# Performance work log

Measured on AMD Instinct MI355X. Metric: run time of the kernel, lower is better.

## Reference

```python
import jax, jax.numpy as jnp
import numpy as np

N, E, G = 50000, 800000, 512
IN, HID, H1, H2, OUT = 128, 32, 8, 4, 128
D1, D2 = HID * H1, HID * H2  # 256, 128


def _ln(x, g, b, eps=1e-5):
    m = x.mean(-1, keepdims=True)
    v = jnp.var(x, axis=-1, keepdims=True)
    return (x - m) * jax.lax.rsqrt(v + eps) * g + b


def _gat_conv(x, W, a_src, a_dst, bias, edge_index, heads, ch, concat):
    # PyG GATConv (eval): h = xW per head; e = leakyrelu(a_src.h_src + a_dst.h_dst);
    # segment softmax over destination nodes; scatter-sum messages; self-loops added.
    n = x.shape[0]
    h = (x @ W).reshape(n, heads, ch)                      # [N,H,C]
    asrc = jnp.sum(h * a_src, axis=-1)                     # [N,H]
    adst = jnp.sum(h * a_dst, axis=-1)                     # [N,H]
    loop = jnp.arange(n)
    src = jnp.concatenate([edge_index[0], loop])           # [E+N]
    dst = jnp.concatenate([edge_index[1], loop])
    e = jax.nn.leaky_relu(asrc[src] + adst[dst], 0.2)      # [E+N,H]
    emax = jax.ops.segment_max(e, dst, num_segments=n)
    p = jnp.exp(e - emax[dst])
    denom = jax.ops.segment_sum(p, dst, num_segments=n)
    alpha = p / (denom[dst] + 1e-16)                       # [E+N,H]
    out = jax.ops.segment_sum(h[src] * alpha[..., None], dst, num_segments=n)  # [N,H,C]
    out = out.reshape(n, heads * ch) if concat else out.mean(axis=1)
    return out + bias


def setup_inputs():
    key = jax.random.key(0)
    ks = jax.random.split(key, 32)
    g = lambda i, shape, s=0.05: jax.random.normal(ks[i], shape, dtype=jnp.float32) * s
    inp = {
        "x": jax.random.normal(ks[0], (N, IN), dtype=jnp.float32),
        "edge_index": jax.random.randint(ks[1], (2, E), 0, N, dtype=jnp.int32),
        "batch": jnp.sort(jax.random.randint(ks[2], (N,), 0, G, dtype=jnp.int32)),
        # GAT layer 1: in 128 -> 8 heads x 32
        "W1": g(3, (IN, H1 * HID)), "a_src1": g(4, (H1, HID)), "a_dst1": g(5, (H1, HID)),
        "b1": jnp.zeros((D1,), jnp.float32), "g1": jnp.ones((D1,), jnp.float32), "be1": jnp.zeros((D1,), jnp.float32),
        "pw1": g(6, (IN, D1)), "pb1": jnp.zeros((D1,), jnp.float32),
        # GAT layer 2: 256 -> 4 heads x 32
        "W2": g(7, (D1, H2 * HID)), "a_src2": g(8, (H2, HID)), "a_dst2": g(9, (H2, HID)),
        "b2": jnp.zeros((D2,), jnp.float32), "g2": jnp.ones((D2,), jnp.float32), "be2": jnp.zeros((D2,), jnp.float32),
        "pw2": g(10, (D1, D2)), "pb2": jnp.zeros((D2,), jnp.float32),
        # GAT layer 3: 128 -> 1 head x 128, concat=False
        "W3": g(11, (D2, OUT)), "a_src3": g(12, (1, OUT)), "a_dst3": g(13, (1, OUT)),
        "b3": jnp.zeros((OUT,), jnp.float32), "g3": jnp.ones((OUT,), jnp.float32), "be3": jnp.zeros((OUT,), jnp.float32),
        "pw3": g(14, (D2, OUT)), "pb3": jnp.zeros((OUT,), jnp.float32),
    }
    return inp


def reference(x, edge_index, batch,
              W1, a_src1, a_dst1, b1, g1, be1, pw1, pb1,
              W2, a_src2, a_dst2, b2, g2, be2, pw2, pb2,
              W3, a_src3, a_dst3, b3, g3, be3, pw3, pb3):
    h1 = _gat_conv(x, W1, a_src1, a_dst1, b1, edge_index, H1, HID, True)
    h1 = jax.nn.elu(_ln(h1, g1, be1) + (x @ pw1 + pb1))
    h2 = _gat_conv(h1, W2, a_src2, a_dst2, b2, edge_index, H2, HID, True)
    h2 = jax.nn.elu(_ln(h2, g2, be2) + (h1 @ pw2 + pb2))
    h3 = _gat_conv(h2, W3, a_src3, a_dst3, b3, edge_index, 1, OUT, False)
    h3 = jax.nn.elu(_ln(h3, g3, be3) + (h2 @ pw3 + pb3))
    # jk='last' -> h3; global mean pool per graph
    sums = jax.ops.segment_sum(h3, batch, num_segments=G)              # [G,OUT]
    cnt = jax.ops.segment_sum(jnp.ones((N,), h3.dtype), batch, num_segments=G)
    return sums / jnp.maximum(cnt, 1.0)[:, None]
```

## Files before the change

kernel.cpp:

```cpp
#include <hip/hip_runtime.h>
#include <math.h>


typedef __bf16 bf16x8 __attribute__((ext_vector_type(8)));
typedef float f32x4 __attribute__((ext_vector_type(4)));

static __device__ __forceinline__ float bf2f(unsigned short u) {
  union { unsigned int i; float f; } c;
  c.i = ((unsigned int)u) << 16;
  return c.f;
}
static __device__ __forceinline__ unsigned short f2bf(float f) {
  __bf16 b = (__bf16)f;
  return __builtin_bit_cast(unsigned short, b);
}
static __device__ __forceinline__ float wave_sum(float v) {
#pragma unroll
  for (int off = 1; off < 64; off <<= 1) v += __shfl_xor(v, off, 64);
  return v;
}
static __device__ __forceinline__ float bflo(unsigned int w) {
  union { unsigned int i; float f; } c;
  c.i = w << 16;
  return c.f;
}
static __device__ __forceinline__ float bfhi(unsigned int w) {
  union { unsigned int i; float f; } c;
  c.i = w & 0xFFFF0000u;
  return c.f;
}

template <int K>
__global__ __launch_bounds__(256) void fused_gemm_kernel(
    const unsigned short* __restrict__ A, const unsigned short* __restrict__ Bp1,
    const unsigned short* __restrict__ Bp2, const float* __restrict__ bias2,
    unsigned short* __restrict__ C1, unsigned short* __restrict__ C2, int Ncols) {
  const int lane = threadIdx.x & 63;
  const int w = threadIdx.x >> 6;
  const int ml = lane & 15, kq = lane >> 4;
  const int row0 = blockIdx.y * 64 + (w >> 1) * 32;
  const int colt0 = blockIdx.x * 4 + (w & 1) * 2;
  constexpr int KB = K / 32;

  f32x4 w00 = {}, w01 = {}, w10 = {}, w11 = {};
  f32x4 p00 = {}, p01 = {}, p10 = {}, p11 = {};
  const unsigned short* a0 = A + (size_t)(row0 + ml) * K + kq * 8;
  const unsigned short* b1 = Bp1 + ((size_t)colt0 * KB * 64 + lane) * 8;
  const unsigned short* b2 = Bp2 + ((size_t)colt0 * KB * 64 + lane) * 8;
#pragma unroll
  for (int kb = 0; kb < KB; kb++) {
    bf16x8 af0 = __builtin_bit_cast(bf16x8, *(const uint4*)(a0 + kb * 32));
    bf16x8 af1 = __builtin_bit_cast(bf16x8, *(const uint4*)(a0 + 16 * K + kb * 32));
    bf16x8 bw0 = __builtin_bit_cast(bf16x8, *(const uint4*)(b1 + (size_t)kb * 512));
    bf16x8 bw1 = __builtin_bit_cast(bf16x8, *(const uint4*)(b1 + (size_t)(KB + kb) * 512));
    bf16x8 bp0 = __builtin_bit_cast(bf16x8, *(const uint4*)(b2 + (size_t)kb * 512));
    bf16x8 bp1 = __builtin_bit_cast(bf16x8, *(const uint4*)(b2 + (size_t)(KB + kb) * 512));
    w00 = __builtin_amdgcn_mfma_f32_16x16x32_bf16(af0, bw0, w00, 0, 0, 0);
    w01 = __builtin_amdgcn_mfma_f32_16x16x32_bf16(af0, bw1, w01, 0, 0, 0);
    w10 = __builtin_amdgcn_mfma_f32_16x16x32_bf16(af1, bw0, w10, 0, 0, 0);
    w11 = __builtin_amdgcn_mfma_f32_16x16x32_bf16(af1, bw1, w11, 0, 0, 0);
    p00 = __builtin_amdgcn_mfma_f32_16x16x32_bf16(af0, bp0, p00, 0, 0, 0);
    p01 = __builtin_amdgcn_mfma_f32_16x16x32_bf16(af0, bp1, p01, 0, 0, 0);
    p10 = __builtin_amdgcn_mfma_f32_16x16x32_bf16(af1, bp0, p10, 0, 0, 0);
    p11 = __builtin_amdgcn_mfma_f32_16x16x32_bf16(af1, bp1, p11, 0, 0, 0);
  }
  const int c0 = colt0 * 16 + ml, c1 = c0 + 16;
  const float bi0 = bias2[c0], bi1 = bias2[c1];
#pragma unroll
  for (int r = 0; r < 4; r++) {
    const size_t rA = (size_t)(row0 + kq * 4 + r);
    const size_t rB = rA + 16;
    C1[rA * Ncols + c0] = f2bf(w00[r]);
    C1[rA * Ncols + c1] = f2bf(w01[r]);
    C1[rB * Ncols + c0] = f2bf(w10[r]);
    C1[rB * Ncols + c1] = f2bf(w11[r]);
    C2[rA * Ncols + c0] = f2bf(p00[r] + bi0);
    C2[rA * Ncols + c1] = f2bf(p01[r] + bi1);
    C2[rB * Ncols + c0] = f2bf(p10[r] + bi0);
    C2[rB * Ncols + c1] = f2bf(p11[r] + bi1);
  }
}

__global__ void repack_b_kernel(const float* __restrict__ B, unsigned short* __restrict__ Bp,
                                int K, int Ncols) {
  const int idx = blockIdx.x * 256 + threadIdx.x;
  const int KB = K >> 5;
  const int total = (Ncols >> 4) * KB * 64;
  if (idx >= total) return;
  const int lane = idx & 63;
  const int kb = (idx >> 6) % KB;
  const int nt = idx / (KB << 6);
  const int ml = lane & 15, kq = lane >> 4;
  unsigned short* dst = Bp + (size_t)idx * 8;
#pragma unroll
  for (int j = 0; j < 8; j++)
    dst[j] = f2bf(B[(size_t)(kb * 32 + kq * 8 + j) * Ncols + nt * 16 + ml]);
}

__global__ void cast_bf16_kernel(const float* __restrict__ src,
                                 unsigned short* __restrict__ dst, int n4) {
  const int i = blockIdx.x * 256 + threadIdx.x;
  if (i >= n4) return;
  float4 v = ((const float4*)src)[i];
  ushort4 o;
  o.x = f2bf(v.x); o.y = f2bf(v.y); o.z = f2bf(v.z); o.w = f2bf(v.w);
  ((ushort4*)dst)[i] = o;
}

template <int H, int C, int VEC>
__global__ __launch_bounds__(256) void attn_kernel(
    const unsigned short* __restrict__ hfeat, const float* __restrict__ a_src,
    const float* __restrict__ a_dst, float* __restrict__ asrc,
    float* __restrict__ adst, int N) {
  const int DOUT = H * C;
  const int wave = threadIdx.x >> 6;
  const int lane = threadIdx.x & 63;
  const int n = blockIdx.x * 4 + wave;
  if (n >= N) return;

  const unsigned short* hr = &hfeat[(size_t)n * DOUT + lane * VEC];
  float hv[VEC], sv[VEC], dv[VEC];
  if constexpr (VEC == 4) {
    ushort4 t = *(const ushort4*)hr;
    hv[0] = bf2f(t.x); hv[1] = bf2f(t.y); hv[2] = bf2f(t.z); hv[3] = bf2f(t.w);
    float4 s = *(const float4*)&a_src[lane * 4];
    sv[0] = s.x; sv[1] = s.y; sv[2] = s.z; sv[3] = s.w;
    float4 d = *(const float4*)&a_dst[lane * 4];
    dv[0] = d.x; dv[1] = d.y; dv[2] = d.z; dv[3] = d.w;
  } else {
    ushort2 t = *(const ushort2*)hr;
    hv[0] = bf2f(t.x); hv[1] = bf2f(t.y);
    float2 s = *(const float2*)&a_src[lane * 2];
    sv[0] = s.x; sv[1] = s.y;
    float2 d = *(const float2*)&a_dst[lane * 2];
    dv[0] = d.x; dv[1] = d.y;
  }
  float ps = 0.f, pd = 0.f;
#pragma unroll
  for (int i = 0; i < VEC; i++) {
    ps += hv[i] * sv[i];
    pd += hv[i] * dv[i];
  }
  const int L = C / VEC;
#pragma unroll
  for (int off = 1; off < L; off <<= 1) {
    ps += __shfl_xor(ps, off, 64);
    pd += __shfl_xor(pd, off, 64);
  }
  if ((lane % L) == 0) {
    const int hh = lane / L;
    asrc[n * H + hh] = ps;
    adst[n * H + hh] = pd;
  }
}

template <int H, int C, int SPLIT>
__global__ __launch_bounds__(256) void gat_agg_kernel(
    const unsigned short* __restrict__ hfeat, const float* __restrict__ asrc,
    const float* __restrict__ adst, const int* __restrict__ rowptr,
    const int* __restrict__ col, const float* __restrict__ bias,
    const float* __restrict__ gamma, const float* __restrict__ beta,
    const unsigned short* __restrict__ proj, unsigned short* __restrict__ out, int N) {
  constexpr int DOUT = H * C;
  constexpr int RL = DOUT / 8;
  constexpr int PD = 4;
  const int wave = threadIdx.x >> 6;
  const int lane = threadIdx.x & 63;
  const int n = blockIdx.x * 4 + wave;
  if (n >= N) return;
  const int rl = lane % RL;
  const int sub = lane / RL;
  const int c0 = rl * 8;
  const int myh = c0 / C;
  const int start = rowptr[n];
  const int deg = rowptr[n + 1] - start;
  const int vlen = deg + 1;
  const float my_adl = adst[n * H + myh];

  float acc[8];
#pragma unroll
  for (int i = 0; i < 8; i++) acc[i] = 0.f;
  float psum = 0.f;

  for (int chunk = 0; chunk < vlen; chunk += 64) {
    const int loc = chunk + lane;
    const int cv = (loc < deg) ? col[start + loc] : n;
    const int m = min(64, vlen - chunk);
    const int steps = (m + SPLIT - 1) / SPLIT;
    const int ngroups = (steps + PD - 1) / PD;

    float aA[PD], aB[PD];
    uint4 hA[PD], hB[PD];

#pragma unroll
    for (int k = 0; k < PD; k++) {
      const int local = k * SPLIT + sub;
      int s = __shfl(cv, local & 63);
      if (local >= m) s = n;
      aA[k] = asrc[s * H + myh];
      hA[k] = *(const uint4*)&hfeat[(size_t)s * DOUT + c0];
    }
    for (int g = 0; g < ngroups; g += 2) {
      if (g + 1 < ngroups) {
#pragma unroll
        for (int k = 0; k < PD; k++) {
          const int local = ((g + 1) * PD + k) * SPLIT + sub;
          int s = __shfl(cv, local & 63);
          if (local >= m) s = n;
          aB[k] = asrc[s * H + myh];
          hB[k] = *(const uint4*)&hfeat[(size_t)s * DOUT + c0];
        }
      }
#pragma unroll
      for (int k = 0; k < PD; k++) {
        const int local = (g * PD + k) * SPLIT + sub;
        float e = aA[k] + my_adl;
        e = (e > 0.f) ? e : 0.2f * e;
        float p = __expf(e);
        p = (local < m) ? p : 0.f;
        psum += p;
        acc[0] += bflo(hA[k].x) * p; acc[1] += bfhi(hA[k].x) * p;
        acc[2] += bflo(hA[k].y) * p; acc[3] += bfhi(hA[k].y) * p;
        acc[4] += bflo(hA[k].z) * p; acc[5] += bfhi(hA[k].z) * p;
        acc[6] += bflo(hA[k].w) * p; acc[7] += bfhi(hA[k].w) * p;
      }
      if (g + 1 < ngroups) {
        if (g + 2 < ngroups) {
#pragma unroll
          for (int k = 0; k < PD; k++) {
            const int local = ((g + 2) * PD + k) * SPLIT + sub;
            int s = __shfl(cv, local & 63);
            if (local >= m) s = n;
            aA[k] = asrc[s * H + myh];
            hA[k] = *(const uint4*)&hfeat[(size_t)s * DOUT + c0];
          }
        }
#pragma unroll
        for (int k = 0; k < PD; k++) {
          const int local = ((g + 1) * PD + k) * SPLIT + sub;
          float e = aB[k] + my_adl;
          e = (e > 0.f) ? e : 0.2f * e;
          float p = __expf(e);
          p = (local < m) ? p : 0.f;
          psum += p;
          acc[0] += bflo(hB[k].x) * p; acc[1] += bfhi(hB[k].x) * p;
          acc[2] += bflo(hB[k].y) * p; acc[3] += bfhi(hB[k].y) * p;
          acc[4] += bflo(hB[k].z) * p; acc[5] += bfhi(hB[k].z) * p;
          acc[6] += bflo(hB[k].w) * p; acc[7] += bfhi(hB[k].w) * p;
        }
      }
    }
  }

#pragma unroll
  for (int o = RL; o < 64; o <<= 1) {
    psum += __shfl_xor(psum, o);
#pragma unroll
    for (int i = 0; i < 8; i++) acc[i] += __shfl_xor(acc[i], o);
  }

  const float rs = 1.f / (psum + 1e-16f);
  const float4 bi0 = *(const float4*)&bias[c0];
  const float4 bi1 = *(const float4*)&bias[c0 + 4];
  float v[8];
  v[0] = acc[0] * rs + bi0.x; v[1] = acc[1] * rs + bi0.y;
  v[2] = acc[2] * rs + bi0.z; v[3] = acc[3] * rs + bi0.w;
  v[4] = acc[4] * rs + bi1.x; v[5] = acc[5] * rs + bi1.y;
  v[6] = acc[6] * rs + bi1.z; v[7] = acc[7] * rs + bi1.w;

  float s8 = 0.f;
#pragma unroll
  for (int i = 0; i < 8; i++) s8 += v[i];
  const float mean = wave_sum(s8) / (float)(DOUT * SPLIT);
  float q8 = 0.f;
#pragma unroll
  for (int i = 0; i < 8; i++) {
    v[i] -= mean;
    q8 += v[i] * v[i];
  }
  const float var = wave_sum(q8) / (float)(DOUT * SPLIT);
  const float rstd = rsqrtf(var + 1e-5f);

  const float4 ga0 = *(const float4*)&gamma[c0];
  const float4 ga1 = *(const float4*)&gamma[c0 + 4];
  const float4 be0 = *(const float4*)&beta[c0];
  const float4 be1 = *(const float4*)&beta[c0 + 4];
  const uint4 pr = *(const uint4*)&proj[(size_t)n * DOUT + c0];
  float o0 = v[0] * rstd * ga0.x + be0.x + bflo(pr.x);
  float o1 = v[1] * rstd * ga0.y + be0.y + bfhi(pr.x);
  float o2 = v[2] * rstd * ga0.z + be0.z + bflo(pr.y);
  float o3 = v[3] * rstd * ga0.w + be0.w + bfhi(pr.y);
  float o4 = v[4] * rstd * ga1.x + be1.x + bflo(pr.z);
  float o5 = v[5] * rstd * ga1.y + be1.y + bfhi(pr.z);
  float o6 = v[6] * rstd * ga1.z + be1.z + bflo(pr.w);
  float o7 = v[7] * rstd * ga1.w + be1.w + bfhi(pr.w);
  o0 = (o0 > 0.f) ? o0 : expm1f(o0);
  o1 = (o1 > 0.f) ? o1 : expm1f(o1);
  o2 = (o2 > 0.f) ? o2 : expm1f(o2);
  o3 = (o3 > 0.f) ? o3 : expm1f(o3);
  o4 = (o4 > 0.f) ? o4 : expm1f(o4);
  o5 = (o5 > 0.f) ? o5 : expm1f(o5);
  o6 = (o6 > 0.f) ? o6 : expm1f(o6);
  o7 = (o7 > 0.f) ? o7 : expm1f(o7);
  if (sub == 0) {
    uint4 ov;
    ov.x = (unsigned int)f2bf(o0) | ((unsigned int)f2bf(o1) << 16);
    ov.y = (unsigned int)f2bf(o2) | ((unsigned int)f2bf(o3) << 16);
    ov.z = (unsigned int)f2bf(o4) | ((unsigned int)f2bf(o5) << 16);
    ov.w = (unsigned int)f2bf(o6) | ((unsigned int)f2bf(o7) << 16);
    *(uint4*)&out[(size_t)n * DOUT + c0] = ov;
  }
}

__global__ void hist_kernel(const int* __restrict__ dst, int* __restrict__ cnt, int E) {
  const int e = blockIdx.x * 256 + threadIdx.x;
  if (e < E) atomicAdd(&cnt[dst[e]], 1);
}

__global__ __launch_bounds__(256) void scan1_kernel(int* __restrict__ cnt,
                                                    int* __restrict__ sums, int N) {
  __shared__ int sm[256];
  const int i = blockIdx.x * 256 + threadIdx.x;
  const int v = (i < N) ? cnt[i] : 0;
  sm[threadIdx.x] = v;
  __syncthreads();
  for (int off = 1; off < 256; off <<= 1) {
    const int t = (threadIdx.x >= off) ? sm[threadIdx.x - off] : 0;
    __syncthreads();
    sm[threadIdx.x] += t;
    __syncthreads();
  }
  if (i < N) cnt[i] = sm[threadIdx.x] - v;
  if (threadIdx.x == 255) sums[blockIdx.x] = sm[255];
}

__global__ __launch_bounds__(256) void scan2_kernel(int* __restrict__ sums, int nb) {
  __shared__ int sm[256];
  const int v = (threadIdx.x < nb) ? sums[threadIdx.x] : 0;
  sm[threadIdx.x] = v;
  __syncthreads();
  for (int off = 1; off < 256; off <<= 1) {
    const int t = (threadIdx.x >= off) ? sm[threadIdx.x - off] : 0;
    __syncthreads();
    sm[threadIdx.x] += t;
    __syncthreads();
  }
  if (threadIdx.x < nb) sums[threadIdx.x] = sm[threadIdx.x] - v;
}

__global__ void scan3_kernel(const int* __restrict__ cnt, const int* __restrict__ sums,
                             int* __restrict__ rowptr, int* __restrict__ cursor,
                             int N, int E) {
  const int i = blockIdx.x * 256 + threadIdx.x;
  if (i < N) {
    const int r = cnt[i] + sums[blockIdx.x];
    rowptr[i] = r;
    cursor[i] = r;
  }
  if (i == 0) rowptr[N] = E;
}

__global__ void scatter_kernel(const int* __restrict__ src, const int* __restrict__ dst,
                               int* __restrict__ cursor, int* __restrict__ col, int E) {
  const int e = blockIdx.x * 256 + threadIdx.x;
  if (e < E) {
    const int p = atomicAdd(&cursor[dst[e]], 1);
    col[p] = src[e];
  }
}

__global__ __launch_bounds__(128) void pool_kernel(const unsigned short* __restrict__ h3,
                                                   const int* __restrict__ batch,
                                                   float* __restrict__ out, int N) {
  __shared__ int sse[2];
  const int g = blockIdx.x;
  if (threadIdx.x == 0) {
    int lo = 0, hi = N;
    while (lo < hi) { const int mid = (lo + hi) >> 1; if (batch[mid] < g) lo = mid + 1; else hi = mid; }
    sse[0] = lo;
    lo = 0; hi = N;
    while (lo < hi) { const int mid = (lo + hi) >> 1; if (batch[mid] < g + 1) lo = mid + 1; else hi = mid; }
    sse[1] = lo;
  }
  __syncthreads();
  const int s = sse[0], e = sse[1];
  float sum = 0.f;
  for (int r = s; r < e; r++) sum += bf2f(h3[(size_t)r * 128 + threadIdx.x]);
  out[g * 128 + threadIdx.x] = (e > s) ? sum / (float)(e - s) : 0.f;
}

extern "C" void kernel_launch(void* const* d_in, const int* in_sizes, int n_in,
                              void* d_out, int out_size, void* d_ws, size_t ws_size,
                              hipStream_t stream) {
  const float* x      = (const float*)d_in[0];
  const int* edge_idx = (const int*)d_in[1];
  const int* batch    = (const int*)d_in[2];
  const float* W1     = (const float*)d_in[3];
  const float* a_src1 = (const float*)d_in[4];
  const float* a_dst1 = (const float*)d_in[5];
  const float* b1     = (const float*)d_in[6];
  const float* g1     = (const float*)d_in[7];
  const float* be1    = (const float*)d_in[8];
  const float* pw1    = (const float*)d_in[9];
  const float* pb1    = (const float*)d_in[10];
  const float* W2     = (const float*)d_in[11];
  const float* a_src2 = (const float*)d_in[12];
  const float* a_dst2 = (const float*)d_in[13];
  const float* b2     = (const float*)d_in[14];
  const float* g2     = (const float*)d_in[15];
  const float* be2    = (const float*)d_in[16];
  const float* pw2    = (const float*)d_in[17];
  const float* pb2    = (const float*)d_in[18];
  const float* W3     = (const float*)d_in[19];
  const float* a_src3 = (const float*)d_in[20];
  const float* a_dst3 = (const float*)d_in[21];
  const float* b3     = (const float*)d_in[22];
  const float* g3     = (const float*)d_in[23];
  const float* be3    = (const float*)d_in[24];
  const float* pw3    = (const float*)d_in[25];
  const float* pb3    = (const float*)d_in[26];

  const int NN = in_sizes[0] / 128;
  const int E  = in_sizes[1] / 2;
  const int G  = out_size / 128;
  const int M64 = (NN + 63) & ~63;

  size_t off = 0;
  auto alloc = [&](size_t bytes) {
    size_t r = off;
    off += (bytes + 255) & ~(size_t)255;
    return r;
  };
  char* ws = (char*)d_ws;
  unsigned short* big0 = (unsigned short*)(ws + alloc((size_t)M64 * 256 * 2));
  unsigned short* big1 = (unsigned short*)(ws + alloc((size_t)M64 * 256 * 2));
  unsigned short* s0   = (unsigned short*)(ws + alloc((size_t)M64 * 128 * 2));
  unsigned short* s1   = (unsigned short*)(ws + alloc((size_t)M64 * 128 * 2));
  unsigned short* projb = (unsigned short*)(ws + alloc((size_t)M64 * 256 * 2));
  float* asrcB = (float*)(ws + alloc((size_t)NN * 8 * 4));
  float* adstB = (float*)(ws + alloc((size_t)NN * 8 * 4));
  int* rowptr  = (int*)(ws + alloc((size_t)(NN + 1) * 4));
  int* cnt     = (int*)(ws + alloc((size_t)NN * 4));
  int* cursor  = (int*)(ws + alloc((size_t)NN * 4));
  int* colb    = (int*)(ws + alloc((size_t)E * 4));
  int* sums    = (int*)(ws + alloc(256 * 4));
  unsigned short* BpW1 = (unsigned short*)(ws + alloc(128 * 256 * 2));
  unsigned short* BpP1 = (unsigned short*)(ws + alloc(128 * 256 * 2));
  unsigned short* BpW2 = (unsigned short*)(ws + alloc(256 * 128 * 2));
  unsigned short* BpP2 = (unsigned short*)(ws + alloc(256 * 128 * 2));
  unsigned short* BpW3 = (unsigned short*)(ws + alloc(128 * 128 * 2));
  unsigned short* BpP3 = (unsigned short*)(ws + alloc(128 * 128 * 2));
  (void)ws_size; (void)n_in;

  const int EB = (E + 255) / 256;
  const int NB = (NN + 255) / 256;
  const int NW = (NN + 3) / 4;
  const int MB = M64 / 64;
  const int pad = M64 - NN;

  hipMemsetAsync(cnt, 0, (size_t)NN * 4, stream);
  hist_kernel<<<EB, 256, 0, stream>>>(edge_idx + E, cnt, E);
  scan1_kernel<<<NB, 256, 0, stream>>>(cnt, sums, NN);
  scan2_kernel<<<1, 256, 0, stream>>>(sums, NB);
  scan3_kernel<<<NB, 256, 0, stream>>>(cnt, sums, rowptr, cursor, NN, E);
  scatter_kernel<<<EB, 256, 0, stream>>>(edge_idx, edge_idx + E, cursor, colb, E);

  cast_bf16_kernel<<<(NN * 128 / 4 + 255) / 256, 256, 0, stream>>>(x, s0, NN * 128 / 4);
  if (pad) {
    hipMemsetAsync(s0 + (size_t)NN * 128, 0, (size_t)pad * 128 * 2, stream);
    hipMemsetAsync(big1 + (size_t)NN * 256, 0, (size_t)pad * 256 * 2, stream);
    hipMemsetAsync(s1 + (size_t)NN * 128, 0, (size_t)pad * 128 * 2, stream);
  }

  repack_b_kernel<<<((256 / 16) * (128 / 32) * 64 + 255) / 256, 256, 0, stream>>>(W1, BpW1, 128, 256);
  repack_b_kernel<<<((256 / 16) * (128 / 32) * 64 + 255) / 256, 256, 0, stream>>>(pw1, BpP1, 128, 256);
  repack_b_kernel<<<((128 / 16) * (256 / 32) * 64 + 255) / 256, 256, 0, stream>>>(W2, BpW2, 256, 128);
  repack_b_kernel<<<((128 / 16) * (256 / 32) * 64 + 255) / 256, 256, 0, stream>>>(pw2, BpP2, 256, 128);
  repack_b_kernel<<<((128 / 16) * (128 / 32) * 64 + 255) / 256, 256, 0, stream>>>(W3, BpW3, 128, 128);
  repack_b_kernel<<<((128 / 16) * (128 / 32) * 64 + 255) / 256, 256, 0, stream>>>(pw3, BpP3, 128, 128);

  fused_gemm_kernel<128><<<dim3(4, MB), 256, 0, stream>>>(s0, BpW1, BpP1, pb1, big0, projb, 256);
  attn_kernel<8, 32, 4><<<NW, 256, 0, stream>>>(big0, a_src1, a_dst1, asrcB, adstB, NN);
  gat_agg_kernel<8, 32, 2><<<NW, 256, 0, stream>>>(big0, asrcB, adstB, rowptr, colb, b1, g1, be1, projb, big1, NN);

  fused_gemm_kernel<256><<<dim3(2, MB), 256, 0, stream>>>(big1, BpW2, BpP2, pb2, s0, projb, 128);
  attn_kernel<4, 32, 2><<<NW, 256, 0, stream>>>(s0, a_src2, a_dst2, asrcB, adstB, NN);
  gat_agg_kernel<4, 32, 4><<<NW, 256, 0, stream>>>(s0, asrcB, adstB, rowptr, colb, b2, g2, be2, projb, s1, NN);

  fused_gemm_kernel<128><<<dim3(2, MB), 256, 0, stream>>>(s1, BpW3, BpP3, pb3, big0, projb, 128);
  attn_kernel<1, 128, 2><<<NW, 256, 0, stream>>>(big0, a_src3, a_dst3, asrcB, adstB, NN);
  gat_agg_kernel<1, 128, 4><<<NW, 256, 0, stream>>>(big0, asrcB, adstB, rowptr, colb, b3, g3, be3, projb, s0, NN);

  pool_kernel<<<G, 128, 0, stream>>>(s0, batch, (float*)d_out, NN);
}
```

Measured before the change: 544.8 us.

## Switch to fp16, fuse attention logits into GEMM, merge setup kernels

Switches the storage and MFMA type from bf16 to fp16 and moves the per-node attention-score computation (a_src/a_dst dot products) into the GEMM epilogue through cross-lane shuffles, with atomics for the single-head layer. This removes three attn_kernel launches and their re-read of the feature matrix. The six weight repacks are merged into one kernel and the memsets into small kernels to cut launch count. Aggregation now accumulates messages with packed half2 FMAs per chunk, which lowers ALU work but risks fp16 precision loss and overflow in the accumulator.

Result: faster. 498.1 us (-8.6%).

```diff
diff --git a/kernel.cpp b/kernel.cpp
--- a/kernel.cpp
+++ b/kernel.cpp
@@ -1,40 +1,36 @@
 #include <hip/hip_runtime.h>
+#include <hip/hip_fp16.h>
 #include <math.h>
 
 
-typedef __bf16 bf16x8 __attribute__((ext_vector_type(8)));
+typedef _Float16 f16x8 __attribute__((ext_vector_type(8)));
 typedef float f32x4 __attribute__((ext_vector_type(4)));
 
-static __device__ __forceinline__ float bf2f(unsigned short u) {
-  union { unsigned int i; float f; } c;
-  c.i = ((unsigned int)u) << 16;
-  return c.f;
-}
-static __device__ __forceinline__ unsigned short f2bf(float f) {
-  __bf16 b = (__bf16)f;
-  return __builtin_bit_cast(unsigned short, b);
+static __device__ __forceinline__ float h2f(unsigned short u) {
+  return __half2float(__builtin_bit_cast(__half, u));
+}
+static __device__ __forceinline__ unsigned short f2h(float f) {
+  return __builtin_bit_cast(unsigned short, __float2half_rn(f));
+}
+static __device__ __forceinline__ float hlo(unsigned int w) {
+  return __low2float(__builtin_bit_cast(__half2, w));
+}
+static __device__ __forceinline__ float hhi(unsigned int w) {
+  return __high2float(__builtin_bit_cast(__half2, w));
 }
 static __device__ __forceinline__ float wave_sum(float v) {
 #pragma unroll
   for (int off = 1; off < 64; off <<= 1) v += __shfl_xor(v, off, 64);
   return v;
 }
-static __device__ __forceinline__ float bflo(unsigned int w) {
-  union { unsigned int i; float f; } c;
-  c.i = w << 16;
-  return c.f;
-}
-static __device__ __forceinline__ float bfhi(unsigned int w) {
-  union { unsigned int i; float f; } c;
-  c.i = w & 0xFFFF0000u;
-  return c.f;
-}
-
-template <int K>
+
+template <int K, int C, int H, bool ATOMIC>
 __global__ __launch_bounds__(256) void fused_gemm_kernel(
     const unsigned short* __restrict__ A, const unsigned short* __restrict__ Bp1,
     const unsigned short* __restrict__ Bp2, const float* __restrict__ bias2,
-    unsigned short* __restrict__ C1, unsigned short* __restrict__ C2, int Ncols) {
+    const float* __restrict__ a_src, const float* __restrict__ a_dst,
+    unsigned short* __restrict__ C1, unsigned short* __restrict__ C2,
+    float* __restrict__ asrc, float* __restrict__ adst, int Ncols) {
   const int lane = threadIdx.x & 63;
   const int w = threadIdx.x >> 6;
   const int ml = lane & 15, kq = lane >> 4;
@@ -49,20 +45,20 @@
   const unsigned short* b2 = Bp2 + ((size_t)colt0 * KB * 64 + lane) * 8;
 #pragma unroll
   for (int kb = 0; kb < KB; kb++) {
-    bf16x8 af0 = __builtin_bit_cast(bf16x8, *(const uint4*)(a0 + kb * 32));
-    bf16x8 af1 = __builtin_bit_cast(bf16x8, *(const uint4*)(a0 + 16 * K + kb * 32));
-    bf16x8 bw0 = __builtin_bit_cast(bf16x8, *(const uint4*)(b1 + (size_t)kb * 512));
-    bf16x8 bw1 = __builtin_bit_cast(bf16x8, *(const uint4*)(b1 + (size_t)(KB + kb) * 512));
-    bf16x8 bp0 = __builtin_bit_cast(bf16x8, *(const uint4*)(b2 + (size_t)kb * 512));
-    bf16x8 bp1 = __builtin_bit_cast(bf16x8, *(const uint4*)(b2 + (size_t)(KB + kb) * 512));
-    w00 = __builtin_amdgcn_mfma_f32_16x16x32_bf16(af0, bw0, w00, 0, 0, 0);
-    w01 = __builtin_amdgcn_mfma_f32_16x16x32_bf16(af0, bw1, w01, 0, 0, 0);
-    w10 = __builtin_amdgcn_mfma_f32_16x16x32_bf16(af1, bw0, w10, 0, 0, 0);
-    w11 = __builtin_amdgcn_mfma_f32_16x16x32_bf16(af1, bw1, w11, 0, 0, 0);
-    p00 = __builtin_amdgcn_mfma_f32_16x16x32_bf16(af0, bp0, p00, 0, 0, 0);
-    p01 = __builtin_amdgcn_mfma_f32_16x16x32_bf16(af0, bp1, p01, 0, 0, 0);
-    p10 = __builtin_amdgcn_mfma_f32_16x16x32_bf16(af1, bp0, p10, 0, 0, 0);
-    p11 = __builtin_amdgcn_mfma_f32_16x16x32_bf16(af1, bp1, p11, 0, 0, 0);
+    f16x8 af0 = __builtin_bit_cast(f16x8, *(const uint4*)(a0 + kb * 32));
+    f16x8 af1 = __builtin_bit_cast(f16x8, *(const uint4*)(a0 + 16 * K + kb * 32));
+    f16x8 bw0 = __builtin_bit_cast(f16x8, *(const uint4*)(b1 + (size_t)kb * 512));
+    f16x8 bw1 = __builtin_bit_cast(f16x8, *(const uint4*)(b1 + (size_t)(KB + kb) * 512));
+    f16x8 bp0 = __builtin_bit_cast(f16x8, *(const uint4*)(b2 + (size_t)kb * 512));
+    f16x8 bp1 = __builtin_bit_cast(f16x8, *(const uint4*)(b2 + (size_t)(KB + kb) * 512));
+    w00 = __builtin_amdgcn_mfma_f32_16x16x32_f16(af0, bw0, w00, 0, 0, 0);
+    w01 = __builtin_amdgcn_mfma_f32_16x16x32_f16(af0, bw1, w01, 0, 0, 0);
+    w10 = __builtin_amdgcn_mfma_f32_16x16x32_f16(af1, bw0, w10, 0, 0, 0);
+    w11 = __builtin_amdgcn_mfma_f32_16x16x32_f16(af1, bw1, w11, 0, 0, 0);
+    p00 = __builtin_amdgcn_mfma_f32_16x16x32_f16(af0, bp0, p00, 0, 0, 0);
+    p01 = __builtin_amdgcn_mfma_f32_16x16x32_f16(af0, bp1, p01, 0, 0, 0);
+    p10 = __builtin_amdgcn_mfma_f32_16x16x32_f16(af1, bp0, p10, 0, 0, 0);
+    p11 = __builtin_amdgcn_mfma_f32_16x16x32_f16(af1, bp1, p11, 0, 0, 0);
   }
   const int c0 = colt0 * 16 + ml, c1 = c0 + 16;
   const float bi0 = bias2[c0], bi1 = bias2[c1];
@@ -70,23 +66,58 @@
   for (int r = 0; r < 4; r++) {
     const size_t rA = (size_t)(row0 + kq * 4 + r);
     const size_t rB = rA + 16;
-    C1[rA * Ncols + c0] = f2bf(w00[r]);
-    C1[rA * Ncols + c1] = f2bf(w01[r]);
-    C1[rB * Ncols + c0] = f2bf(w10[r]);
-    C1[rB * Ncols + c1] = f2bf(w11[r]);
-    C2[rA * Ncols + c0] = f2bf(p00[r] + bi0);
-    C2[rA * Ncols + c1] = f2bf(p01[r] + bi1);
-    C2[rB * Ncols + c0] = f2bf(p10[r] + bi0);
-    C2[rB * Ncols + c1] = f2bf(p11[r] + bi1);
-  }
-}
-
-__global__ void repack_b_kernel(const float* __restrict__ B, unsigned short* __restrict__ Bp,
-                                int K, int Ncols) {
-  const int idx = blockIdx.x * 256 + threadIdx.x;
+    C1[rA * Ncols + c0] = f2h(w00[r]);
+    C1[rA * Ncols + c1] = f2h(w01[r]);
+    C1[rB * Ncols + c0] = f2h(w10[r]);
+    C1[rB * Ncols + c1] = f2h(w11[r]);
+    C2[rA * Ncols + c0] = f2h(p00[r] + bi0);
+    C2[rA * Ncols + c1] = f2h(p01[r] + bi1);
+    C2[rB * Ncols + c0] = f2h(p10[r] + bi0);
+    C2[rB * Ncols + c1] = f2h(p11[r] + bi1);
+  }
+
+  const int hh = (colt0 * 16) / C;
+  const float aS0 = a_src[hh * C + (c0 % C)], aS1 = a_src[hh * C + (c1 % C)];
+  const float aD0 = a_dst[hh * C + (c0 % C)], aD1 = a_dst[hh * C + (c1 % C)];
+  float pS0[4], pD0[4], pS1[4], pD1[4];
+#pragma unroll
+  for (int r = 0; r < 4; r++) {
+    pS0[r] = w00[r] * aS0 + w01[r] * aS1;
+    pD0[r] = w00[r] * aD0 + w01[r] * aD1;
+    pS1[r] = w10[r] * aS0 + w11[r] * aS1;
+    pD1[r] = w10[r] * aD0 + w11[r] * aD1;
+  }
+#pragma unroll
+  for (int off = 1; off < 16; off <<= 1) {
+#pragma unroll
+    for (int r = 0; r < 4; r++) {
+      pS0[r] += __shfl_xor(pS0[r], off);
+      pD0[r] += __shfl_xor(pD0[r], off);
+      pS1[r] += __shfl_xor(pS1[r], off);
+      pD1[r] += __shfl_xor(pD1[r], off);
+    }
+  }
+  if (ml < 4) {
+    const int r = ml;
+    const int rowA = row0 + kq * 4 + r;
+    const int rowB = rowA + 16;
+    if constexpr (ATOMIC) {
+      atomicAdd(&asrc[rowA * H + hh], pS0[r]);
+      atomicAdd(&adst[rowA * H + hh], pD0[r]);
+      atomicAdd(&asrc[rowB * H + hh], pS1[r]);
+      atomicAdd(&adst[rowB * H + hh], pD1[r]);
+    } else {
+      asrc[rowA * H + hh] = pS0[r];
+      adst[rowA * H + hh] = pD0[r];
+      asrc[rowB * H + hh] = pS1[r];
+      adst[rowB * H + hh] = pD1[r];
+    }
+  }
+}
+
+static __device__ __forceinline__ void repack_one(const float* B, unsigned short* Bp,
+                                                  int K, int Ncols, int idx) {
   const int KB = K >> 5;
-  const int total = (Ncols >> 4) * KB * 64;
-  if (idx >= total) return;
   const int lane = idx & 63;
   const int kb = (idx >> 6) % KB;
   const int nt = idx / (KB << 6);
@@ -94,64 +125,51 @@
   unsigned short* dst = Bp + (size_t)idx * 8;
 #pragma unroll
   for (int j = 0; j < 8; j++)
-    dst[j] = f2bf(B[(size_t)(kb * 32 + kq * 8 + j) * Ncols + nt * 16 + ml]);
-}
-
-__global__ void cast_bf16_kernel(const float* __restrict__ src,
-                                 unsigned short* __restrict__ dst, int n4) {
+    dst[j] = f2h(B[(size_t)(kb * 32 + kq * 8 + j) * Ncols + nt * 16 + ml]);
+}
+
+__global__ __launch_bounds__(256) void repack_all_kernel(
+    const float* W1, const float* pw1, const float* W2, const float* pw2,
+    const float* W3, const float* pw3, unsigned short* BpW1, unsigned short* BpP1,
+    unsigned short* BpW2, unsigned short* BpP2, unsigned short* BpW3,
+    unsigned short* BpP3) {
+  int idx = blockIdx.x * 256 + threadIdx.x;
+  if (idx < 4096) { repack_one(W1, BpW1, 128, 256, idx); return; }
+  idx -= 4096;
+  if (idx < 4096) { repack_one(pw1, BpP1, 128, 256, idx); return; }
+  idx -= 4096;
+  if (idx < 4096) { repack_one(W2, BpW2, 256, 128, idx); return; }
+  idx -= 4096;
+  if (idx < 4096) { repack_one(pw2, BpP2, 256, 128, idx); return; }
+  idx -= 4096;
+  if (idx < 2048) { repack_one(W3, BpW3, 128, 128, idx); return; }
+  idx -= 2048;
+  repack_one(pw3, BpP3, 128, 128, idx);
+}
+
+__global__ void cast_f16_kernel(const float* __restrict__ src,
+                                unsigned short* __restrict__ dst, int n4, int pad4) {
   const int i = blockIdx.x * 256 + threadIdx.x;
-  if (i >= n4) return;
-  float4 v = ((const float4*)src)[i];
+  if (i >= n4 + pad4) return;
   ushort4 o;
-  o.x = f2bf(v.x); o.y = f2bf(v.y); o.z = f2bf(v.z); o.w = f2bf(v.w);
+  if (i < n4) {
+    float4 v = ((const float4*)src)[i];
+    o.x = f2h(v.x); o.y = f2h(v.y); o.z = f2h(v.z); o.w = f2h(v.w);
+  } else {
+    o.x = o.y = o.z = o.w = 0;
+  }
   ((ushort4*)dst)[i] = o;
 }
 
-template <int H, int C, int VEC>
-__global__ __launch_bounds__(256) void attn_kernel(
-    const unsigned short* __restrict__ hfeat, const float* __restrict__ a_src,
-    const float* __restrict__ a_dst, float* __restrict__ asrc,
-    float* __restrict__ adst, int N) {
-  const int DOUT = H * C;
-  const int wave = threadIdx.x >> 6;
-  const int lane = threadIdx.x & 63;
-  const int n = blockIdx.x * 4 + wave;
-  if (n >= N) return;
-
-  const unsigned short* hr = &hfeat[(size_t)n * DOUT + lane * VEC];
-  float hv[VEC], sv[VEC], dv[VEC];
-  if constexpr (VEC == 4) {
-    ushort4 t = *(const ushort4*)hr;
-    hv[0] = bf2f(t.x); hv[1] = bf2f(t.y); hv[2] = bf2f(t.z); hv[3] = bf2f(t.w);
-    float4 s = *(const float4*)&a_src[lane * 4];
-    sv[0] = s.x; sv[1] = s.y; sv[2] = s.z; sv[3] = s.w;
-    float4 d = *(const float4*)&a_dst[lane * 4];
-    dv[0] = d.x; dv[1] = d.y; dv[2] = d.z; dv[3] = d.w;
-  } else {
-    ushort2 t = *(const ushort2*)hr;
-    hv[0] = bf2f(t.x); hv[1] = bf2f(t.y);
-    float2 s = *(const float2*)&a_src[lane * 2];
-    sv[0] = s.x; sv[1] = s.y;
-    float2 d = *(const float2*)&a_dst[lane * 2];
-    dv[0] = d.x; dv[1] = d.y;
-  }
-  float ps = 0.f, pd = 0.f;
-#pragma unroll
-  for (int i = 0; i < VEC; i++) {
-    ps += hv[i] * sv[i];
-    pd += hv[i] * dv[i];
-  }
-  const int L = C / VEC;
-#pragma unroll
-  for (int off = 1; off < L; off <<= 1) {
-    ps += __shfl_xor(ps, off, 64);
-    pd += __shfl_xor(pd, off, 64);
-  }
-  if ((lane % L) == 0) {
-    const int hh = lane / L;
-    asrc[n * H + hh] = ps;
-    adst[n * H + hh] = pd;
-  }
+__global__ void zero_pads_kernel(unsigned short* b256, unsigned short* b128, int pad) {
+  const int i = blockIdx.x * 256 + threadIdx.x;
+  if (i < pad * 256) b256[i] = 0;
+  if (i < pad * 128) b128[i] = 0;
+}
+
+__global__ void zero2_kernel(float* a, float* b, int n) {
+  const int i = blockIdx.x * 256 + threadIdx.x;
+  if (i < n) { a[i] = 0.f; b[i] = 0.f; }
 }
 
 template <int H, int C, int SPLIT>
@@ -181,6 +199,7 @@
 #pragma unroll
   for (int i = 0; i < 8; i++) acc[i] = 0.f;
   float psum = 0.f;
+  const __half2 hz = __float2half2_rn(0.f);
 
   for (int chunk = 0; chunk < vlen; chunk += 64) {
     const int loc = chunk + lane;
@@ -189,6 +208,7 @@
     const int steps = (m + SPLIT - 1) / SPLIT;
     const int ngroups = (steps + PD - 1) / PD;
 
+    __half2 acc2[4] = {hz, hz, hz, hz};
     float aA[PD], aB[PD];
     uint4 hA[PD], hB[PD];
 
@@ -219,10 +239,11 @@
         float p = __expf(e);
         p = (local < m) ? p : 0.f;
         psum += p;
-        acc[0] += bflo(hA[k].x) * p; acc[1] += bfhi(hA[k].x) * p;
-        acc[2] += bflo(hA[k].y) * p; acc[3] += bfhi(hA[k].y) * p;
-        acc[4] += bflo(hA[k].z) * p; acc[5] += bfhi(hA[k].z) * p;
-        acc[6] += bflo(hA[k].w) * p; acc[7] += bfhi(hA[k].w) * p;
+        const __half2 pp = __float2half2_rn(p);
+        acc2[0] = __hfma2(__builtin_bit_cast(__half2, hA[k].x), pp, acc2[0]);
+        acc2[1] = __hfma2(__builtin_bit_cast(__half2, hA[k].y), pp, acc2[1]);
+        acc2[2] = __hfma2(__builtin_bit_cast(__half2, hA[k].z), pp, acc2[2]);
+        acc2[3] = __hfma2(__builtin_bit_cast(__half2, hA[k].w), pp, acc2[3]);
       }
       if (g + 1 < ngroups) {
         if (g + 2 < ngroups) {
@@ -243,12 +264,18 @@
           float p = __expf(e);
           p = (local < m) ? p : 0.f;
           psum += p;
-          acc[0] += bflo(hB[k].x) * p; acc[1] += bfhi(hB[k].x) * p;
-          acc[2] += bflo(hB[k].y) * p; acc[3] += bfhi(hB[k].y) * p;
-          acc[4] += bflo(hB[k].z) * p; acc[5] += bfhi(hB[k].z) * p;
-          acc[6] += bflo(hB[k].w) * p; acc[7] += bfhi(hB[k].w) * p;
+          const __half2 pp = __float2half2_rn(p);
+          acc2[0] = __hfma2(__builtin_bit_cast(__half2, hB[k].x), pp, acc2[0]);
+          acc2[1] = __hfma2(__builtin_bit_cast(__half2, hB[k].y), pp, acc2[1]);
+          acc2[2] = __hfma2(__builtin_bit_cast(__half2, hB[k].z), pp, acc2[2]);
+          acc2[3] = __hfma2(__builtin_bit_cast(__half2, hB[k].w), pp, acc2[3]);
         }
       }
+    }
+#pragma unroll
+    for (int i = 0; i < 4; i++) {
+      acc[2 * i] += __low2float(acc2[i]);
+      acc[2 * i + 1] += __high2float(acc2[i]);
     }
   }
 
@@ -286,14 +313,14 @@
   const float4 be0 = *(const float4*)&beta[c0];
   const float4 be1 = *(const float4*)&beta[c0 + 4];
   const uint4 pr = *(const uint4*)&proj[(size_t)n * DOUT + c0];
-  float o0 = v[0] * rstd * ga0.x + be0.x + bflo(pr.x);
-  float o1 = v[1] * rstd * ga0.y + be0.y + bfhi(pr.x);
-  float o2 = v[2] * rstd * ga0.z + be0.z + bflo(pr.y);
-  float o3 = v[3] * rstd * ga0.w + be0.w + bfhi(pr.y);
-  float o4 = v[4] * rstd * ga1.x + be1.x + bflo(pr.z);
-  float o5 = v[5] * rstd * ga1.y + be1.y + bfhi(pr.z);
-  float o6 = v[6] * rstd * ga1.z + be1.z + bflo(pr.w);
-  float o7 = v[7] * rstd * ga1.w + be1.w + bfhi(pr.w);
+  float o0 = v[0] * rstd * ga0.x + be0.x + hlo(pr.x);
+  float o1 = v[1] * rstd * ga0.y + be0.y + hhi(pr.x);
+  float o2 = v[2] * rstd * ga0.z + be0.z + hlo(pr.y);
+  float o3 = v[3] * rstd * ga0.w + be0.w + hhi(pr.y);
+  float o4 = v[4] * rstd * ga1.x + be1.x + hlo(pr.z);
+  float o5 = v[5] * rstd * ga1.y + be1.y + hhi(pr.z);
+  float o6 = v[6] * rstd * ga1.z + be1.z + hlo(pr.w);
+  float o7 = v[7] * rstd * ga1.w + be1.w + hhi(pr.w);
   o0 = (o0 > 0.f) ? o0 : expm1f(o0);
   o1 = (o1 > 0.f) ? o1 : expm1f(o1);
   o2 = (o2 > 0.f) ? o2 : expm1f(o2);
@@ -304,10 +331,10 @@
   o7 = (o7 > 0.f) ? o7 : expm1f(o7);
   if (sub == 0) {
     uint4 ov;
-    ov.x = (unsigned int)f2bf(o0) | ((unsigned int)f2bf(o1) << 16);
-    ov.y = (unsigned int)f2bf(o2) | ((unsigned int)f2bf(o3) << 16);
-    ov.z = (unsigned int)f2bf(o4) | ((unsigned int)f2bf(o5) << 16);
-    ov.w = (unsigned int)f2bf(o6) | ((unsigned int)f2bf(o7) << 16);
+    ov.x = (unsigned int)f2h(o0) | ((unsigned int)f2h(o1) << 16);
+    ov.y = (unsigned int)f2h(o2) | ((unsigned int)f2h(o3) << 16);
+    ov.z = (unsigned int)f2h(o4) | ((unsigned int)f2h(o5) << 16);
+    ov.w = (unsigned int)f2h(o6) | ((unsigned int)f2h(o7) << 16);
     *(uint4*)&out[(size_t)n * DOUT + c0] = ov;
   }
 }
@@ -385,7 +412,7 @@
   __syncthreads();
   const int s = sse[0], e = sse[1];
   float sum = 0.f;
-  for (int r = s; r < e; r++) sum += bf2f(h3[(size_t)r * 128 + threadIdx.x]);
+  for (int r = s; r < e; r++) sum += h2f(h3[(size_t)r * 128 + threadIdx.x]);
   out[g * 128 + threadIdx.x] = (e > s) ? sum / (float)(e - s) : 0.f;
 }
 
@@ -437,8 +464,8 @@
   unsigned short* s0   = (unsigned short*)(ws + alloc((size_t)M64 * 128 * 2));
   unsigned short* s1   = (unsigned short*)(ws + alloc((size_t)M64 * 128 * 2));
   unsigned short* projb = (unsigned short*)(ws + alloc((size_t)M64 * 256 * 2));
-  float* asrcB = (float*)(ws + alloc((size_t)NN * 8 * 4));
-  float* adstB = (float*)(ws + alloc((size_t)NN * 8 * 4));
+  float* asrcB = (float*)(ws + alloc((size_t)M64 * 8 * 4));
+  float* adstB = (float*)(ws + alloc((size_t)M64 * 8 * 4));
   int* rowptr  = (int*)(ws + alloc((size_t)(NN + 1) * 4));
   int* cnt     = (int*)(ws + alloc((size_t)NN * 4));
   int* cursor  = (int*)(ws + alloc((size_t)NN * 4));
@@ -465,31 +492,29 @@
   scan3_kernel<<<NB, 256, 0, stream>>>(cnt, sums, rowptr, cursor, NN, E);
   scatter_kernel<<<EB, 256, 0, stream>>>(edge_idx, edge_idx + E, cursor, colb, E);
 
-  cast_bf16_kernel<<<(NN * 128 / 4 + 255) / 256, 256, 0, stream>>>(x, s0, NN * 128 / 4);
-  if (pad) {
-    hipMemsetAsync(s0 + (size_t)NN * 128, 0, (size_t)pad * 128 * 2, stream);
-    hipMemsetAsync(big1 + (size_t)NN * 256, 0, (size_t)pad * 256 * 2, stream);
-    hipMemsetAsync(s1 + (size_t)NN * 128, 0, (size_t)pad * 128 * 2, stream);
-  }
-
-  repack_b_kernel<<<((256 / 16) * (128 / 32) * 64 + 255) / 256, 256, 0, stream>>>(W1, BpW1, 128, 256);
-  repack_b_kernel<<<((256 / 16) * (128 / 32) * 64 + 255) / 256, 256, 0, stream>>>(pw1, BpP1, 128, 256);
-  repack_b_kernel<<<((128 / 16) * (256 / 32) * 64 + 255) / 256, 256, 0, stream>>>(W2, BpW2, 256, 128);
-  repack_b_kernel<<<((128 / 16) * (256 / 32) * 64 + 255) / 256, 256, 0, stream>>>(pw2, BpP2, 256, 128);
-  repack_b_kernel<<<((128 / 16) * (128 / 32) * 64 + 255) / 256, 256, 0, stream>>>(W3, BpW3, 128, 128);
-  repack_b_kernel<<<((128 / 16) * (128 / 32) * 64 + 255) / 256, 256, 0, stream>>>(pw3, BpP3, 128, 128);
-
-  fused_gemm_kernel<128><<<dim3(4, MB), 256, 0, stream>>>(s0, BpW1, BpP1, pb1, big0, projb, 256);
-  attn_kernel<8, 32, 4><<<NW, 256, 0, stream>>>(big0, a_src1, a_dst1, asrcB, adstB, NN);
-  gat_agg_kernel<8, 32, 2><<<NW, 256, 0, stream>>>(big0, asrcB, adstB, rowptr, colb, b1, g1, be1, projb, big1, NN);
-
-  fused_gemm_kernel<256><<<dim3(2, MB), 256, 0, stream>>>(big1, BpW2, BpP2, pb2, s0, projb, 128);
-  attn_kernel<4, 32, 2><<<NW, 256, 0, stream>>>(s0, a_src2, a_dst2, asrcB, adstB, NN);
-  gat_agg_kernel<4, 32, 4><<<NW, 256, 0, stream>>>(s0, asrcB, adstB, rowptr, colb, b2, g2, be2, projb, s1, NN);
-
-  fused_gemm_kernel<128><<<dim3(2, MB), 256, 0, stream>>>(s1, BpW3, BpP3, pb3, big0, projb, 128);
-  attn_kernel<1, 128, 2><<<NW, 256, 0, stream>>>(big0, a_src3, a_dst3, asrcB, adstB, NN);
-  gat_agg_kernel<1, 128, 4><<<NW, 256, 0, stream>>>(big0, asrcB, adstB, rowptr, colb, b3, g3, be3, projb, s0, NN);
+  cast_f16_kernel<<<(M64 * 128 / 4 + 255) / 256, 256, 0, stream>>>(x, s0, NN * 32, pad * 32);
+  if (pad)
+    zero_pads_kernel<<<(pad * 256 + 255) / 256, 256, 0, stream>>>(
+        big1 + (size_t)NN * 256, s1 + (size_t)NN * 128, pad);
+
+  repack_all_kernel<<<80, 256, 0, stream>>>(W1, pw1, W2, pw2, W3, pw3,
+                                            BpW1, BpP1, BpW2, BpP2, BpW3, BpP3);
+
+  fused_gemm_kernel<128, 32, 8, false><<<dim3(4, MB), 256, 0, stream>>>(
+      s0, BpW1, BpP1, pb1, a_src1, a_dst1, big0, projb, asrcB, adstB, 256);
+  gat_agg_kernel<8, 32, 2><<<NW, 256, 0, stream>>>(big0, asrcB, adstB, rowptr, colb,
+                                                   b1, g1, be1, projb, big1, NN);
+
+  fused_gemm_kernel<256, 32, 4, false><<<dim3(2, MB), 256, 0, stream>>>(
+      big1, BpW2, BpP2, pb2, a_src2, a_dst2, s0, projb, asrcB, adstB, 128);
+  gat_agg_kernel<4, 32, 4><<<NW, 256, 0, stream>>>(s0, asrcB, adstB, rowptr, colb,
+                                                   b2, g2, be2, projb, s1, NN);
+
+  zero2_kernel<<<(M64 + 255) / 256, 256, 0, stream>>>(asrcB, adstB, M64);
+  fused_gemm_kernel<128, 128, 1, true><<<dim3(2, MB), 256, 0, stream>>>(
+      s1, BpW3, BpP3, pb3, a_src3, a_dst3, big0, projb, asrcB, adstB, 128);
+  gat_agg_kernel<1, 128, 4><<<NW, 256, 0, stream>>>(big0, asrcB, adstB, rowptr, colb,
+                                                    b3, g3, be3, projb, s0, NN);
 
   pool_kernel<<<G, 128, 0, stream>>>(s0, batch, (float*)d_out, NN);
 }
```
